# Optimization experiments

Hardware: AMD Instinct MI355X
Metric: run time of the kernel (lower is better)

Reference implementation:

```python
import jax, jax.numpy as jnp
import numpy as np

B, T, R = 512, 4096, 16


def setup_inputs() -> dict:
    key = jax.random.key(0)
    k1, k2, k3 = jax.random.split(key, 3)
    pred = jax.random.normal(k1, (B, T, R), dtype=jnp.float32)
    target = jax.random.normal(k2, (B, T, R), dtype=jnp.float32)
    # replicate_mask marks a contiguous prefix of valid replicates (matches
    # the original `pred[b, :, :n_valid]` slicing). Lengths in [0, R].
    lengths = jax.random.randint(k3, (B,), 0, R + 1)
    replicate_mask = (jnp.arange(R)[None, :] < lengths[:, None]).astype(jnp.float32)
    return {"pred": pred, "target": target, "replicate_mask": replicate_mask}


def _masked_var_unbiased(x, m, n_safe):
    # x: [B,T,R], m: [B,1,R], n_safe: [B,1] (clamped >= 2)
    mean = jnp.sum(x * m, axis=-1, keepdims=True) / n_safe[:, :, None]  # [B,T,1]
    sq = jnp.sum(((x - mean) ** 2) * m, axis=-1)  # [B,T]
    return sq / (n_safe - 1.0)  # unbiased (torch var default ddof=1)


def reference(pred, target, replicate_mask):
    weight = 0.1
    n = jnp.sum(replicate_mask, axis=-1)  # [B]
    n_safe = jnp.maximum(n, 2.0)[:, None]  # avoid div-by-zero; masked out below
    m = replicate_mask[:, None, :]  # [B,1,R]
    pred_var = _masked_var_unbiased(pred, m, n_safe)      # [B,T]
    target_var = _masked_var_unbiased(target, m, n_safe)  # [B,T]
    mse = jnp.mean((pred_var - target_var) ** 2, axis=-1)  # [B]
    valid = n > 1.0
    n_multi = jnp.sum(valid.astype(jnp.float32))
    total = jnp.sum(jnp.where(valid, mse, 0.0))
    loss = jnp.where(n_multi > 0, total / jnp.maximum(n_multi, 1.0), 0.0)
    return weight * loss
```

## Files before the change

### kernel.cpp

```cpp
#include <hip/hip_runtime.h>

#define B_DIM 512
#define T_DIM 4096
#define NSLOT 256
#define BLOCKS 8192
#define THREADS 256
#define ITER 4

__device__ __forceinline__ float hsum4(float4 v) { return (v.x + v.y) + (v.z + v.w); }

__device__ __forceinline__ float mdot(float4 x, float4 m) {
    return (x.x * m.x + x.y * m.y) + (x.z * m.z + x.w * m.w);
}

__device__ __forceinline__ float msq(float4 x, float4 m, float mu) {
    float a = x.x - mu, b = x.y - mu, c = x.z - mu, d = x.w - mu;
    return (a * a * m.x + b * b * m.y) + (c * c * m.z + d * d * m.w);
}

__global__ __launch_bounds__(THREADS) void rcl_main(
    const float4* __restrict__ pred4, const float4* __restrict__ targ4,
    const float4* __restrict__ mask4, double* __restrict__ slots)
{
    const int tid0 = blockIdx.x * THREADS + threadIdx.x;

    float4 mv[ITER], pv[ITER], qv[ITER];
#pragma unroll
    for (int i = 0; i < ITER; i++) {
        const int g = tid0 + i * (BLOCKS * THREADS);
        const int row = g >> 2;
        const int part = g & 3;
        const int b = row >> 12;
        mv[i] = mask4[(b << 2) + part];
        pv[i] = pred4[g];
        qv[i] = targ4[g];
    }

    float csum = 0.0f;
#pragma unroll
    for (int i = 0; i < ITER; i++) {
        float n = hsum4(mv[i]);
        n += __shfl_xor(n, 1, 64);
        n += __shfl_xor(n, 2, 64);

        float sp = mdot(pv[i], mv[i]);
        sp += __shfl_xor(sp, 1, 64);
        sp += __shfl_xor(sp, 2, 64);
        float sq = mdot(qv[i], mv[i]);
        sq += __shfl_xor(sq, 1, 64);
        sq += __shfl_xor(sq, 2, 64);

        float nsafe = fmaxf(n, 2.0f);
        float mean_p = sp / nsafe;
        float mean_q = sq / nsafe;

        float vd = msq(pv[i], mv[i], mean_p) - msq(qv[i], mv[i], mean_q);
        vd += __shfl_xor(vd, 1, 64);
        vd += __shfl_xor(vd, 2, 64);

        float dd = vd / (nsafe - 1.0f);
        csum += (n > 1.0f) ? dd * dd * 0.25f : 0.0f;
    }

    for (int off = 32; off > 0; off >>= 1)
        csum += __shfl_down(csum, off, 64);

    __shared__ float partial[THREADS / 64];
    const int lane = threadIdx.x & 63;
    const int w = threadIdx.x >> 6;
    if (lane == 0) partial[w] = csum;
    __syncthreads();
    if (threadIdx.x == 0) {
        float s = (partial[0] + partial[1]) + (partial[2] + partial[3]);
        atomicAdd(&slots[blockIdx.x & (NSLOT - 1)], (double)s);
    }
}

__global__ __launch_bounds__(256) void rcl_final(
    const double* __restrict__ slots, const float4* __restrict__ mask4,
    float* __restrict__ out)
{
    __shared__ double dred[256];
    __shared__ float fred[256];
    const int t = threadIdx.x;

    double tot = slots[t];

    float cnt = 0.0f;
    for (int bb = t; bb < B_DIM; bb += 256) {
        const float4* mp = mask4 + (bb << 2);
        float nn = (hsum4(mp[0]) + hsum4(mp[1])) + (hsum4(mp[2]) + hsum4(mp[3]));
        cnt += (nn > 1.0f) ? 1.0f : 0.0f;
    }

    dred[t] = tot;
    fred[t] = cnt;
    __syncthreads();
    for (int s = 128; s > 0; s >>= 1) {
        if (t < s) { dred[t] += dred[t + s]; fred[t] += fred[t + s]; }
        __syncthreads();
    }
    if (t == 0) {
        double nm = (double)fred[0];
        out[0] = (nm > 0.0) ? (float)(0.1 * (dred[0] / ((double)T_DIM * nm))) : 0.0f;
    }
}

extern "C" void kernel_launch(void* const* d_in, const int* in_sizes, int n_in,
                              void* d_out, int out_size, void* d_ws, size_t ws_size,
                              hipStream_t stream) {
    const float4* pred4 = (const float4*)d_in[0];
    const float4* targ4 = (const float4*)d_in[1];
    const float4* mask4 = (const float4*)d_in[2];
    float* out = (float*)d_out;

    double* slots = (double*)d_ws;

    hipMemsetAsync(d_ws, 0, NSLOT * sizeof(double), stream);
    rcl_main<<<BLOCKS, THREADS, 0, stream>>>(pred4, targ4, mask4, slots);
    rcl_final<<<1, 256, 0, stream>>>(slots, mask4, out);
}
```

Before: 278.3 us.

## Use one-pass variance with DPP quad reductions and more work per thread

Replaces the two-pass masked variance (compute the mean, then the squared deviations) with a single pass that computes n*sum(x^2) - sum(x)^2. This removes the serial dependency on the mean. The cross-lane quad sums now use DPP quad_perm instead of ds_swizzle/bpermute shuffles, and the grid is halved while each thread handles twice as many float4 rows. The one-pass formula can lose precision through cancellation when the mean is large relative to the variance.

```diff
diff --git a/kernel.cpp b/kernel.cpp
--- a/kernel.cpp
+++ b/kernel.cpp
@@ -3,9 +3,9 @@
 #define B_DIM 512
 #define T_DIM 4096
 #define NSLOT 256
-#define BLOCKS 8192
+#define BLOCKS 4096
 #define THREADS 256
-#define ITER 4
+#define ITER 8
 
 __device__ __forceinline__ float hsum4(float4 v) { return (v.x + v.y) + (v.z + v.w); }
 
@@ -13,9 +13,16 @@
     return (x.x * m.x + x.y * m.y) + (x.z * m.z + x.w * m.w);
 }
 
-__device__ __forceinline__ float msq(float4 x, float4 m, float mu) {
-    float a = x.x - mu, b = x.y - mu, c = x.z - mu, d = x.w - mu;
-    return (a * a * m.x + b * b * m.y) + (c * c * m.z + d * d * m.w);
+__device__ __forceinline__ float mdot2(float4 x, float4 m) {
+    return (x.x * x.x * m.x + x.y * x.y * m.y) + (x.z * x.z * m.z + x.w * x.w * m.w);
+}
+
+__device__ __forceinline__ float qsum(float v) {
+    int t = __builtin_amdgcn_update_dpp(0, __float_as_int(v), 0xB1, 0xF, 0xF, true);
+    v += __int_as_float(t);
+    t = __builtin_amdgcn_update_dpp(0, __float_as_int(v), 0x4E, 0xF, 0xF, true);
+    v += __int_as_float(t);
+    return v;
 }
 
 __global__ __launch_bounds__(THREADS) void rcl_main(
@@ -28,38 +35,25 @@
 #pragma unroll
     for (int i = 0; i < ITER; i++) {
         const int g = tid0 + i * (BLOCKS * THREADS);
-        const int row = g >> 2;
-        const int part = g & 3;
-        const int b = row >> 12;
-        mv[i] = mask4[(b << 2) + part];
         pv[i] = pred4[g];
         qv[i] = targ4[g];
+        mv[i] = mask4[((g >> 14) << 2) + (g & 3)];
     }
 
     float csum = 0.0f;
 #pragma unroll
     for (int i = 0; i < ITER; i++) {
-        float n = hsum4(mv[i]);
-        n += __shfl_xor(n, 1, 64);
-        n += __shfl_xor(n, 2, 64);
-
-        float sp = mdot(pv[i], mv[i]);
-        sp += __shfl_xor(sp, 1, 64);
-        sp += __shfl_xor(sp, 2, 64);
-        float sq = mdot(qv[i], mv[i]);
-        sq += __shfl_xor(sq, 1, 64);
-        sq += __shfl_xor(sq, 2, 64);
+        const float4 m = mv[i], p = pv[i], q = qv[i];
+        float n   = qsum(hsum4(m));
+        float sp  = qsum(mdot(p, m));
+        float sp2 = qsum(mdot2(p, m));
+        float sq  = qsum(mdot(q, m));
+        float sq2 = qsum(mdot2(q, m));
 
         float nsafe = fmaxf(n, 2.0f);
-        float mean_p = sp / nsafe;
-        float mean_q = sq / nsafe;
-
-        float vd = msq(pv[i], mv[i], mean_p) - msq(qv[i], mv[i], mean_q);
-        vd += __shfl_xor(vd, 1, 64);
-        vd += __shfl_xor(vd, 2, 64);
-
-        float dd = vd / (nsafe - 1.0f);
-        csum += (n > 1.0f) ? dd * dd * 0.25f : 0.0f;
+        float inv = 1.0f / (nsafe * (nsafe - 1.0f));
+        float d = ((nsafe * sp2 - sp * sp) - (nsafe * sq2 - sq * sq)) * inv;
+        csum += (n > 1.0f) ? d * d * 0.25f : 0.0f;
     }
 
     for (int off = 32; off > 0; off >>= 1)
```

After: 290.5 us. 4.4% more time.
